# Kernel tuning notes

Hardware: AMD Instinct MI355X
Metric: run time of the kernel (lower is better)

Reference implementation:

```python
import jax, jax.numpy as jnp
import numpy as np

NX = NY = 2048
DT = 0.01
DX = 1.0
DY = 1.0
RE = 1.0
NLEVEL = int(np.log2(NY)) + 1  # 12 levels


def pad_zero(x):
    # Dirichlet (zero) halo of width 1: matches boundary_condition_u/v/k/cw
    return jnp.pad(x, ((0, 0), (0, 0), (1, 1), (1, 1)))


def pad_edge(x):
    # Edge-replicate halo (incl. corners): matches boundary_condition_p
    return jnp.pad(x, ((0, 0), (0, 0), (1, 1), (1, 1)), mode='edge')


def conv2d(x, w, stride=1):
    return jax.lax.conv_general_dilated(
        x, w, (stride, stride), 'VALID',
        dimension_numbers=('NCHW', 'OIHW', 'NCHW'))


def upsample2(x):
    return jnp.repeat(jnp.repeat(x, 2, axis=2), 2, axis=3)


def pg_vector(u, v, pad_u, pad_v, k1, ADx_u, ADy_u, ADx_v, ADy_v, AD2_u, AD2_v, w_diff):
    # Petrov-Galerkin dissipation. pad_u/pad_v are the padded ORIGINAL velocities:
    # the torch code references the global values_uu/values_vv buffers here.
    k_u = 0.25 * DX * jnp.abs(0.5 * DX ** -3 * (jnp.abs(u) * DX + jnp.abs(v) * DY) * AD2_u) \
        / (0.001 + (jnp.abs(ADx_u) * DX ** -3 + jnp.abs(ADy_u) * DX ** -3) / 2.0)
    k_v = 0.25 * DY * jnp.abs(0.5 * DX ** -3 * (jnp.abs(u) * DX + jnp.abs(v) * DY) * AD2_v) \
        / (0.001 + (jnp.abs(ADx_v) * DX ** -3 + jnp.abs(ADy_v) * DX ** -3) / 2.0)
    k_u = jnp.minimum(k_u, k1)
    k_v = jnp.minimum(k_v, k1)
    k_uu = pad_zero(k_u)
    k_vv = pad_zero(k_v)
    k_x = 1.5 * (k_u * AD2_u + conv2d(pad_u * k_uu, w_diff) - u * conv2d(k_uu, w_diff))
    k_y = 1.5 * (k_v * AD2_v + conv2d(pad_v * k_vv, w_diff) - v * conv2d(k_vv, w_diff))
    return k_x, k_y


def f_cycle_mg(pad_u, pad_v, values_p, iteration, w_A, w_res, w_xadv, w_yadv):
    diag = w_A[0, 0, 1, 1]
    b = -(conv2d(pad_u, w_xadv) + conv2d(pad_v, w_yadv)) / DT
    w = jnp.zeros((1, 1, 2, 2), values_p.dtype)
    r = b
    for _ in range(iteration):
        w = jnp.zeros((1, 1, 2, 2), values_p.dtype)
        r = conv2d(pad_edge(values_p), w_A) - b
        r_s = [r]
        for _i in range(1, NLEVEL - 1):
            r = conv2d(r, w_res, stride=2)  # restriction down to 2x2
            r_s.append(r)
        for i in reversed(range(1, NLEVEL - 1)):
            w = w - conv2d(pad_zero(w), w_A) / diag + r_s[i] / diag  # Jacobi smooth
            w = upsample2(w)  # prolongation
        values_p = values_p - w
        values_p = values_p - conv2d(pad_edge(values_p), w_A) / diag + b / diag
    return values_p, w, r


def setup_inputs() -> dict:
    key = jax.random.key(0)
    ku, kv, kp = jax.random.split(key, 3)
    shp = (1, 1, NY, NX)
    f32 = jnp.float32
    values_u = jax.random.normal(ku, shp, f32) * 0.1
    values_v = jax.random.normal(kv, shp, f32) * 0.1
    values_p = jax.random.normal(kp, shp, f32) * 0.1
    Fx = jnp.zeros(shp, f32)
    Fy = jnp.zeros(shp, f32)
    k1 = jnp.ones(shp, f32) * (DX ** 2 / DT)
    # FD stencils (learned conv params in the torch module)
    w_xadv = jnp.array([[0., 0., 0.], [-0.5, 0., 0.5], [0., 0., 0.]], f32).reshape(1, 1, 3, 3) / DX
    w_yadv = jnp.array([[0., -0.5, 0.], [0., 0., 0.], [0., 0.5, 0.]], f32).reshape(1, 1, 3, 3) / DY
    lap = jnp.array([[0., 1., 0.], [1., -4., 1.], [0., 1., 0.]], f32).reshape(1, 1, 3, 3) / DX ** 2
    w_diff = lap
    w_A = lap  # diag = -4
    w_res = jnp.full((1, 1, 2, 2), 0.25, f32)
    return dict(values_u=values_u, values_v=values_v, values_p=values_p,
                Fx=Fx, Fy=Fy, k1=k1,
                w_xadv=w_xadv, w_yadv=w_yadv, w_diff=w_diff, w_A=w_A, w_res=w_res,
                iteration=5)


def reference(values_u, values_v, values_p, Fx, Fy, k1,
              w_xadv, w_yadv, w_diff, w_A, w_res, iteration):
    pad_u = pad_zero(values_u)
    pad_v = pad_zero(values_v)
    pad_p = pad_edge(values_p)
    Grapx_p = conv2d(pad_p, w_xadv) * DT
    Grapy_p = conv2d(pad_p, w_yadv) * DT
    ADx_u = conv2d(pad_u, w_xadv); ADy_u = conv2d(pad_u, w_yadv)
    ADx_v = conv2d(pad_v, w_xadv); ADy_v = conv2d(pad_v, w_yadv)
    AD2_u = conv2d(pad_u, w_diff); AD2_v = conv2d(pad_v, w_diff)
    k_x, k_y = pg_vector(values_u, values_v, pad_u, pad_v, k1,
                         ADx_u, ADy_u, ADx_v, ADy_v, AD2_u, AD2_v, w_diff)
    b_u = values_u + 0.5 * (RE * k_x * DT - values_u * ADx_u * DT - values_v * ADy_u * DT) - Grapx_p - Fx * DT * 0
    b_v = values_v + 0.5 * (RE * k_y * DT - values_u * ADx_v * DT - values_v * ADy_v * DT) - Grapy_p - Fy * DT * 0
    pad_bu = pad_zero(b_u)
    pad_bv = pad_zero(b_v)
    ADx_u = conv2d(pad_bu, w_xadv); ADy_u = conv2d(pad_bu, w_yadv)
    ADx_v = conv2d(pad_bv, w_xadv); ADy_v = conv2d(pad_bv, w_yadv)
    AD2_u = conv2d(pad_bu, w_diff); AD2_v = conv2d(pad_bv, w_diff)
    # torch code closes over the global padded ORIGINAL velocities here (pad_u, pad_v)
    k_x, k_y = pg_vector(b_u, b_v, pad_u, pad_v, k1,
                         ADx_u, ADy_u, ADx_v, ADy_v, AD2_u, AD2_v, w_diff)
    values_u = values_u + RE * k_x * DT - b_u * ADx_u * DT - b_v * ADy_u * DT - Grapx_p - Fx * DT
    values_v = values_v + RE * k_y * DT - b_u * ADx_v * DT - b_v * ADy_v * DT - Grapy_p - Fy * DT
    values_p, w, r = f_cycle_mg(pad_zero(values_u), pad_zero(values_v), values_p,
                                iteration, w_A, w_res, w_xadv, w_yadv)
    pad_p2 = pad_edge(values_p)
    values_u = values_u - conv2d(pad_p2, w_xadv) * DT
    values_v = values_v - conv2d(pad_p2, w_yadv) * DT
    return values_u, values_v, values_p, w, r
```

## Files before the change

kernel.cpp:

```cpp
#include <hip/hip_runtime.h>

#define NN 2048
#define NN2 (NN * NN)

__device__ __forceinline__ void load6z(const float* __restrict__ A, int i, int j0, float a[6]) {
    if ((unsigned)i >= (unsigned)NN) {
#pragma unroll
        for (int q = 0; q < 6; ++q) a[q] = 0.f;
        return;
    }
    const float* row = A + (size_t)i * NN;
    float4 c = *reinterpret_cast<const float4*>(row + j0);
    a[1] = c.x; a[2] = c.y; a[3] = c.z; a[4] = c.w;
    a[0] = (j0 > 0) ? row[j0 - 1] : 0.f;
    a[5] = (j0 + 4 < NN) ? row[j0 + 4] : 0.f;
}
__device__ __forceinline__ void load4z(const float* __restrict__ A, int i, int j0, float a[4]) {
    if ((unsigned)i >= (unsigned)NN) {
#pragma unroll
        for (int q = 0; q < 4; ++q) a[q] = 0.f;
        return;
    }
    float4 c = *reinterpret_cast<const float4*>(A + (size_t)i * NN + j0);
    a[0] = c.x; a[1] = c.y; a[2] = c.z; a[3] = c.w;
}
__device__ __forceinline__ void load6e(const float* __restrict__ A, int i, int j0, float a[6]) {
    i = i < 0 ? 0 : (i > NN - 1 ? NN - 1 : i);
    const float* row = A + (size_t)i * NN;
    float4 c = *reinterpret_cast<const float4*>(row + j0);
    a[1] = c.x; a[2] = c.y; a[3] = c.z; a[4] = c.w;
    a[0] = (j0 > 0) ? row[j0 - 1] : c.x;
    a[5] = (j0 + 4 < NN) ? row[j0 + 4] : c.w;
}
__device__ __forceinline__ void load4e(const float* __restrict__ A, int i, int j0, float a[4]) {
    i = i < 0 ? 0 : (i > NN - 1 ? NN - 1 : i);
    float4 c = *reinterpret_cast<const float4*>(A + (size_t)i * NN + j0);
    a[0] = c.x; a[1] = c.y; a[2] = c.z; a[3] = c.w;
}
__device__ __forceinline__ void store4(float* __restrict__ A, int i, int j0, const float a[4]) {
    *reinterpret_cast<float4*>(A + (size_t)i * NN + j0) = make_float4(a[0], a[1], a[2], a[3]);
}

__global__ __launch_bounds__(256) void k_pred_f(const float* __restrict__ u, const float* __restrict__ v,
                                                const float* __restrict__ k1, const float* __restrict__ p,
                                                float* __restrict__ bu, float* __restrict__ bv) {
    const float DT = 0.01f;
    __shared__ __align__(16) float su[20][72], sv[20][72];
    __shared__ float sku[18][68], skv[18][68];
    const int jb = blockIdx.x * 64;
    const int ib = blockIdx.y * 16;
    const int tid = threadIdx.y * 16 + threadIdx.x;

    for (int idx = tid; idx < 20 * 18; idx += 256) {
        int r = idx / 18, c4 = idx - r * 18;
        int gi = ib - 2 + r;
        int gj = jb - 4 + c4 * 4;
        float4 uu = make_float4(0.f, 0.f, 0.f, 0.f), vv = uu;
        if ((unsigned)gi < (unsigned)NN) {
            if (gj >= 0 && gj + 3 < NN) {
                uu = *reinterpret_cast<const float4*>(u + (size_t)gi * NN + gj);
                vv = *reinterpret_cast<const float4*>(v + (size_t)gi * NN + gj);
            } else {
                float tu[4], tv[4];
#pragma unroll
                for (int q = 0; q < 4; ++q) {
                    int g = gj + q;
                    bool in = (unsigned)g < (unsigned)NN;
                    tu[q] = in ? u[(size_t)gi * NN + g] : 0.f;
                    tv[q] = in ? v[(size_t)gi * NN + g] : 0.f;
                }
                uu = make_float4(tu[0], tu[1], tu[2], tu[3]);
                vv = make_float4(tv[0], tv[1], tv[2], tv[3]);
            }
        }
        *reinterpret_cast<float4*>(&su[r][c4 * 4]) = uu;
        *reinterpret_cast<float4*>(&sv[r][c4 * 4]) = vv;
    }
    __syncthreads();

    for (int idx = tid; idx < 18 * 66; idx += 256) {
        int r = idx / 66, c = idx - r * 66;
        int gi = ib - 1 + r, gj = jb - 1 + c;
        float kuo = 0.f, kvo = 0.f;
        if ((unsigned)gi < (unsigned)NN && (unsigned)gj < (unsigned)NN) {
            int lr = r + 1, lc = c + 3;
            float uc = su[lr][lc], ul = su[lr][lc - 1], ur = su[lr][lc + 1], ut = su[lr - 1][lc], ub = su[lr + 1][lc];
            float vc = sv[lr][lc], vl = sv[lr][lc - 1], vr = sv[lr][lc + 1], vt = sv[lr - 1][lc], vb = sv[lr + 1][lc];
            float ADxu = 0.5f * (ur - ul), ADyu = 0.5f * (ub - ut);
            float ADxv = 0.5f * (vr - vl), ADyv = 0.5f * (vb - vt);
            float Lu = ul + ur + ut + ub - 4.f * uc;
            float Lv = vl + vr + vt + vb - 4.f * vc;
            float s = fabsf(uc) + fabsf(vc);
            float kuv = 0.25f * fabsf(0.5f * s * Lu) / (0.001f + 0.5f * (fabsf(ADxu) + fabsf(ADyu)));
            float kvv = 0.25f * fabsf(0.5f * s * Lv) / (0.001f + 0.5f * (fabsf(ADxv) + fabsf(ADyv)));
            float k1c = k1[(size_t)gi * NN + gj];
            kuo = fminf(kuv, k1c);
            kvo = fminf(kvv, k1c);
        }
        sku[r][c] = kuo;
        skv[r][c] = kvo;
    }
    __syncthreads();

    const int i = ib + threadIdx.y;
    const int j0 = jb + threadIdx.x * 4;
    float p6[6], pu[4], pd[4], obu[4], obv[4];
    load6e(p, i, j0, p6); load4e(p, i - 1, j0, pu); load4e(p, i + 1, j0, pd);
    const int lur = threadIdx.y + 2, lkr = threadIdx.y + 1;
#pragma unroll
    for (int c = 0; c < 4; ++c) {
        int luc = threadIdx.x * 4 + c + 4, lkc = threadIdx.x * 4 + c + 1;
        float uc = su[lur][luc], ul = su[lur][luc - 1], ur = su[lur][luc + 1], ut = su[lur - 1][luc], ub = su[lur + 1][luc];
        float vc = sv[lur][luc], vl = sv[lur][luc - 1], vr = sv[lur][luc + 1], vt = sv[lur - 1][luc], vb = sv[lur + 1][luc];
        float kuc = sku[lkr][lkc], kul = sku[lkr][lkc - 1], kur = sku[lkr][lkc + 1], kut = sku[lkr - 1][lkc], kub = sku[lkr + 1][lkc];
        float kvc = skv[lkr][lkc], kvl = skv[lkr][lkc - 1], kvr = skv[lkr][lkc + 1], kvt = skv[lkr - 1][lkc], kvb = skv[lkr + 1][lkc];
        float ADxu = 0.5f * (ur - ul), ADyu = 0.5f * (ub - ut);
        float ADxv = 0.5f * (vr - vl), ADyv = 0.5f * (vb - vt);
        float Lu = ul + ur + ut + ub - 4.f * uc;
        float Lv = vl + vr + vt + vb - 4.f * vc;
        float Lku = kul + kur + kut + kub - 4.f * kuc;
        float Lkv = kvl + kvr + kvt + kvb - 4.f * kvc;
        float Luku = ul * kul + ur * kur + ut * kut + ub * kub - 4.f * uc * kuc;
        float Lvkv = vl * kvl + vr * kvr + vt * kvt + vb * kvb - 4.f * vc * kvc;
        float kx = 1.5f * (kuc * Lu + Luku - uc * Lku);
        float ky = 1.5f * (kvc * Lv + Lvkv - vc * Lkv);
        float Grapx = 0.5f * (p6[c + 2] - p6[c]) * DT;
        float Grapy = 0.5f * (pd[c] - pu[c]) * DT;
        obu[c] = uc + 0.5f * (kx * DT - uc * ADxu * DT - vc * ADyu * DT) - Grapx;
        obv[c] = vc + 0.5f * (ky * DT - uc * ADxv * DT - vc * ADyv * DT) - Grapy;
    }
    store4(bu, i, j0, obu);
    store4(bv, i, j0, obv);
}

__global__ __launch_bounds__(256) void k_corr_f(const float* __restrict__ u, const float* __restrict__ v,
                                                const float* __restrict__ k1, const float* __restrict__ p,
                                                const float* __restrict__ bu, const float* __restrict__ bv,
                                                const float* __restrict__ Fx, const float* __restrict__ Fy,
                                                float* __restrict__ un, float* __restrict__ vn) {
    const float DT = 0.01f;
    __shared__ __align__(16) float sbu[20][72], sbv[20][72];
    __shared__ float sku[18][68], skv[18][68];
    const int jb = blockIdx.x * 64;
    const int ib = blockIdx.y * 16;
    const int tid = threadIdx.y * 16 + threadIdx.x;

    for (int idx = tid; idx < 20 * 18; idx += 256) {
        int r = idx / 18, c4 = idx - r * 18;
        int gi = ib - 2 + r;
        int gj = jb - 4 + c4 * 4;
        float4 uu = make_float4(0.f, 0.f, 0.f, 0.f), vv = uu;
        if ((unsigned)gi < (unsigned)NN) {
            if (gj >= 0 && gj + 3 < NN) {
                uu = *reinterpret_cast<const float4*>(bu + (size_t)gi * NN + gj);
                vv = *reinterpret_cast<const float4*>(bv + (size_t)gi * NN + gj);
            } else {
                float tu[4], tv[4];
#pragma unroll
                for (int q = 0; q < 4; ++q) {
                    int g = gj + q;
                    bool in = (unsigned)g < (unsigned)NN;
                    tu[q] = in ? bu[(size_t)gi * NN + g] : 0.f;
                    tv[q] = in ? bv[(size_t)gi * NN + g] : 0.f;
                }
                uu = make_float4(tu[0], tu[1], tu[2], tu[3]);
                vv = make_float4(tv[0], tv[1], tv[2], tv[3]);
            }
        }
        *reinterpret_cast<float4*>(&sbu[r][c4 * 4]) = uu;
        *reinterpret_cast<float4*>(&sbv[r][c4 * 4]) = vv;
    }
    __syncthreads();

    for (int idx = tid; idx < 18 * 66; idx += 256) {
        int r = idx / 66, c = idx - r * 66;
        int gi = ib - 1 + r, gj = jb - 1 + c;
        float kuo = 0.f, kvo = 0.f;
        if ((unsigned)gi < (unsigned)NN && (unsigned)gj < (unsigned)NN) {
            int lr = r + 1, lc = c + 3;
            float uc = sbu[lr][lc], ul = sbu[lr][lc - 1], ur = sbu[lr][lc + 1], ut = sbu[lr - 1][lc], ub = sbu[lr + 1][lc];
            float vc = sbv[lr][lc], vl = sbv[lr][lc - 1], vr = sbv[lr][lc + 1], vt = sbv[lr - 1][lc], vb = sbv[lr + 1][lc];
            float ADxu = 0.5f * (ur - ul), ADyu = 0.5f * (ub - ut);
            float ADxv = 0.5f * (vr - vl), ADyv = 0.5f * (vb - vt);
            float Lu = ul + ur + ut + ub - 4.f * uc;
            float Lv = vl + vr + vt + vb - 4.f * vc;
            float s = fabsf(uc) + fabsf(vc);
            float kuv = 0.25f * fabsf(0.5f * s * Lu) / (0.001f + 0.5f * (fabsf(ADxu) + fabsf(ADyu)));
            float kvv = 0.25f * fabsf(0.5f * s * Lv) / (0.001f + 0.5f * (fabsf(ADxv) + fabsf(ADyv)));
            float k1c = k1[(size_t)gi * NN + gj];
            kuo = fminf(kuv, k1c);
            kvo = fminf(kvv, k1c);
        }
        sku[r][c] = kuo;
        skv[r][c] = kvo;
    }
    __syncthreads();

    const int i = ib + threadIdx.y;
    const int j0 = jb + threadIdx.x * 4;
    float p6[6], pu[4], pd[4];
    float u6[6], uu[4], ud[4], v6[6], vu[4], vd[4], fx[4], fy[4], oun[4], ovn[4];
    load6e(p, i, j0, p6); load4e(p, i - 1, j0, pu); load4e(p, i + 1, j0, pd);
    load6z(u, i, j0, u6); load4z(u, i - 1, j0, uu); load4z(u, i + 1, j0, ud);
    load6z(v, i, j0, v6); load4z(v, i - 1, j0, vu); load4z(v, i + 1, j0, vd);
    load4z(Fx, i, j0, fx); load4z(Fy, i, j0, fy);
    const int lbr = threadIdx.y + 2, lkr = threadIdx.y + 1;
#pragma unroll
    for (int c = 0; c < 4; ++c) {
        int lbc = threadIdx.x * 4 + c + 4, lkc = threadIdx.x * 4 + c + 1;
        float buc = sbu[lbr][lbc], bul = sbu[lbr][lbc - 1], bur = sbu[lbr][lbc + 1], but = sbu[lbr - 1][lbc], bub = sbu[lbr + 1][lbc];
        float bvc = sbv[lbr][lbc], bvl = sbv[lbr][lbc - 1], bvr = sbv[lbr][lbc + 1], bvt = sbv[lbr - 1][lbc], bvb = sbv[lbr + 1][lbc];
        float kuc = sku[lkr][lkc], kul = sku[lkr][lkc - 1], kur = sku[lkr][lkc + 1], kut = sku[lkr - 1][lkc], kub = sku[lkr + 1][lkc];
        float kvc = skv[lkr][lkc], kvl = skv[lkr][lkc - 1], kvr = skv[lkr][lkc + 1], kvt = skv[lkr - 1][lkc], kvb = skv[lkr + 1][lkc];
        float uc = u6[c + 1], ul = u6[c], ur = u6[c + 2], ut = uu[c], ub = ud[c];
        float vc = v6[c + 1], vl = v6[c], vr = v6[c + 2], vt = vu[c], vb = vd[c];
        float ADxbu = 0.5f * (bur - bul), ADybu = 0.5f * (bub - but);
        float ADxbv = 0.5f * (bvr - bvl), ADybv = 0.5f * (bvb - bvt);
        float Lbu = bul + bur + but + bub - 4.f * buc;
        float Lbv = bvl + bvr + bvt + bvb - 4.f * bvc;
        float Lku = kul + kur + kut + kub - 4.f * kuc;
        float Lkv = kvl + kvr + kvt + kvb - 4.f * kvc;
        float Luku = ul * kul + ur * kur + ut * kut + ub * kub - 4.f * uc * kuc;
        float Lvkv = vl * kvl + vr * kvr + vt * kvt + vb * kvb - 4.f * vc * kvc;
        float kx = 1.5f * (kuc * Lbu + Luku - buc * Lku);
        float ky = 1.5f * (kvc * Lbv + Lvkv - bvc * Lkv);
        float Grapx = 0.5f * (p6[c + 2] - p6[c]) * DT;
        float Grapy = 0.5f * (pd[c] - pu[c]) * DT;
        oun[c] = uc + kx * DT - buc * ADxbu * DT - bvc * ADybu * DT - Grapx - fx[c] * DT;
        ovn[c] = vc + ky * DT - buc * ADxbv * DT - bvc * ADybv * DT - Grapy - fy[c] * DT;
    }
    store4(un, i, j0, oun);
    store4(vn, i, j0, ovn);
}

__global__ __launch_bounds__(256) void k_rhs_res(const float* __restrict__ un, const float* __restrict__ vn,
                                                 const float* __restrict__ p, float* __restrict__ b,
                                                 float* __restrict__ r1024, float* __restrict__ r512,
                                                 float* __restrict__ r256) {
    __shared__ float s512r[4][64];
    int tx = threadIdx.x, ty = threadIdx.y;
    int jt = blockIdx.x * 64 + tx;
    int it = blockIdx.y * 4 + ty;
    int j0 = jt * 4, i0 = it * 4;
    float bb[4][4];
#pragma unroll
    for (int r = 0; r < 4; ++r) {
        float u6[6], vu[4], vd[4];
        load6z(un, i0 + r, j0, u6);
        load4z(vn, i0 + r - 1, j0, vu);
        load4z(vn, i0 + r + 1, j0, vd);
#pragma unroll
        for (int c = 0; c < 4; ++c)
            bb[r][c] = -100.f * (0.5f * (u6[c + 2] - u6[c]) + 0.5f * (vd[c] - vu[c]));
        store4(b, i0 + r, j0, bb[r]);
    }
    float p6[6][6];
#pragma unroll
    for (int r = 0; r < 6; ++r) load6e(p, i0 - 1 + r, j0, p6[r]);
    float res[4][4];
#pragma unroll
    for (int r = 0; r < 4; ++r)
#pragma unroll
        for (int c = 0; c < 4; ++c) {
            float pc = p6[r + 1][c + 1];
            res[r][c] = p6[r][c + 1] + p6[r + 2][c + 1] + p6[r + 1][c] + p6[r + 1][c + 2] - 4.f * pc - bb[r][c];
        }
    float q00 = 0.25f * (res[0][0] + res[0][1] + res[1][0] + res[1][1]);
    float q01 = 0.25f * (res[0][2] + res[0][3] + res[1][2] + res[1][3]);
    float q10 = 0.25f * (res[2][0] + res[2][1] + res[3][0] + res[3][1]);
    float q11 = 0.25f * (res[2][2] + res[2][3] + res[3][2] + res[3][3]);
    int ci = it * 2, cj = jt * 2;
    *reinterpret_cast<float2*>(r1024 + (size_t)ci * 1024 + cj)       = make_float2(q00, q01);
    *reinterpret_cast<float2*>(r1024 + (size_t)(ci + 1) * 1024 + cj) = make_float2(q10, q11);
    float s = 0.25f * (q00 + q01 + q10 + q11);
    r512[(size_t)it * 512 + jt] = s;
    s512r[ty][tx] = s;
    __syncthreads();
    int tid = ty * 64 + tx;
    if (tid < 64) {
        int a = tid >> 5, c = tid & 31;
        float m = 0.25f * (s512r[2 * a][2 * c] + s512r[2 * a][2 * c + 1] + s512r[2 * a + 1][2 * c] + s512r[2 * a + 1][2 * c + 1]);
        r256[(size_t)(blockIdx.y * 2 + a) * 256 + blockIdx.x * 32 + c] = m;
    }
}

__global__ __launch_bounds__(1024) void k_small2(const float* __restrict__ r256in,
                                                 float* __restrict__ r128g,
                                                 float* __restrict__ w128_out,
                                                 float* __restrict__ r2_out) {
    __shared__ float sr128[128 * 128];
    __shared__ float sr64[64 * 64];
    __shared__ float sr32[32 * 32];
    __shared__ float sr16[16 * 16];
    __shared__ float sr8[8 * 8];
    __shared__ float sr4[16];
    __shared__ float sr2[4];
    __shared__ float wa[64 * 64];
    __shared__ float wb[64 * 64];
    int t = threadIdx.x;

    for (int idx = t; idx < 128 * 128; idx += 1024) {
        int i = idx >> 7, j = idx & 127;
        const float* s0 = r256in + (2 * i) * 256 + 2 * j;
        float m = 0.25f * (s0[0] + s0[1] + s0[256] + s0[257]);
        sr128[idx] = m;
        r128g[idx] = m;
    }
    __syncthreads();
    for (int idx = t; idx < 64 * 64; idx += 1024) {
        int i = idx >> 6, j = idx & 63;
        const float* s0 = sr128 + (2 * i) * 128 + 2 * j;
        sr64[idx] = 0.25f * (s0[0] + s0[1] + s0[128] + s0[129]);
    }
    __syncthreads();
    if (t < 32 * 32) {
        int i = t >> 5, j = t & 31;
        const float* s0 = sr64 + (2 * i) * 64 + 2 * j;
        sr32[t] = 0.25f * (s0[0] + s0[1] + s0[64] + s0[65]);
    }
    __syncthreads();
    if (t < 16 * 16) {
        int i = t >> 4, j = t & 15;
        const float* s0 = sr32 + (2 * i) * 32 + 2 * j;
        sr16[t] = 0.25f * (s0[0] + s0[1] + s0[32] + s0[33]);
    }
    __syncthreads();
    if (t < 64) {
        int i = t >> 3, j = t & 7;
        const float* s0 = sr16 + (2 * i) * 16 + 2 * j;
        sr8[t] = 0.25f * (s0[0] + s0[1] + s0[16] + s0[17]);
    }
    __syncthreads();
    if (t < 16) {
        int i = t >> 2, j = t & 3;
        const float* s0 = sr8 + (2 * i) * 8 + 2 * j;
        sr4[t] = 0.25f * (s0[0] + s0[1] + s0[8] + s0[9]);
    }
    __syncthreads();
    if (t < 4) {
        int i = t >> 1, j = t & 1;
        const float* s0 = sr4 + (2 * i) * 4 + 2 * j;
        sr2[t] = 0.25f * (s0[0] + s0[1] + s0[4] + s0[5]);
        r2_out[t] = sr2[t];
        float ws = -0.25f * sr2[t];
        wa[(2 * i) * 4 + 2 * j] = ws;
        wa[(2 * i) * 4 + 2 * j + 1] = ws;
        wa[(2 * i + 1) * 4 + 2 * j] = ws;
        wa[(2 * i + 1) * 4 + 2 * j + 1] = ws;
    }
    __syncthreads();

    auto step = [&](const float* win, const float* rl, float* wout, int s) {
        for (int idx = t; idx < s * s; idx += 1024) {
            int i = idx / s, j = idx - i * s;
            float up = i > 0 ? win[(i - 1) * s + j] : 0.f;
            float dn = i < s - 1 ? win[(i + 1) * s + j] : 0.f;
            float lf = j > 0 ? win[i * s + j - 1] : 0.f;
            float rt = j < s - 1 ? win[i * s + j + 1] : 0.f;
            float ws = 0.25f * (up + dn + lf + rt - rl[idx]);
            int o = 2 * s;
            wout[(2 * i) * o + 2 * j] = ws;
            wout[(2 * i) * o + 2 * j + 1] = ws;
            wout[(2 * i + 1) * o + 2 * j] = ws;
            wout[(2 * i + 1) * o + 2 * j + 1] = ws;
        }
    };
    step(wa, sr4, wb, 4);
    __syncthreads();
    step(wb, sr8, wa, 8);
    __syncthreads();
    step(wa, sr16, wb, 16);
    __syncthreads();
    step(wb, sr32, wa, 32);
    __syncthreads();
    step(wa, sr64, w128_out, 64);
}

__global__ __launch_bounds__(256) void k_prolong2(const float* __restrict__ w128, const float* __restrict__ r128,
                                                  const float* __restrict__ r256, float* __restrict__ w512) {
    __shared__ float sw[5][68];
    __shared__ float s128[3][66];
    __shared__ float s256[2][128];
    const int jb = blockIdx.x * 256;
    const int ob = blockIdx.y * 4;
    const int by = blockIdx.y;
    const int rw = by - 2, cw = jb / 4 - 2;
    const int rs = by - 1, cs = jb / 4 - 1;
    const int tid = threadIdx.y * 64 + threadIdx.x;

    for (int idx = tid; idx < 5 * 68; idx += 256) {
        int r = idx / 68, c = idx - r * 68;
        int x = rw + r, y = cw + c;
        sw[r][c] = ((unsigned)x < 128u && (unsigned)y < 128u) ? w128[x * 128 + y] : 0.f;
    }
    __syncthreads();
    if (tid < 3 * 66) {
        int r = tid / 66, c = tid - (tid / 66) * 66;
        int x = rs + r, y = cs + c;
        float val = 0.f;
        if ((unsigned)x < 128u && (unsigned)y < 128u) {
            int lr = r + 1, lc = c + 1;
            val = 0.25f * (sw[lr - 1][lc] + sw[lr + 1][lc] + sw[lr][lc - 1] + sw[lr][lc + 1] - r128[x * 128 + y]);
        }
        s128[r][c] = val;
    }
    __syncthreads();
    {
        int rr = tid >> 7, cc = tid & 127;
        int X = 2 * by + rr, Y = jb / 2 + cc;
        float s = 0.f;
        if (X > 0)   s += s128[((X - 1) >> 1) - rs][(Y >> 1) - cs];
        if (X < 255) s += s128[((X + 1) >> 1) - rs][(Y >> 1) - cs];
        if (Y > 0)   s += s128[(X >> 1) - rs][((Y - 1) >> 1) - cs];
        if (Y < 255) s += s128[(X >> 1) - rs][((Y + 1) >> 1) - cs];
        s256[rr][cc] = 0.25f * (s - r256[X * 256 + Y]);
    }
    __syncthreads();
    const int i = ob + threadIdx.y;
    const int j0 = jb + threadIdx.x * 4;
    const int lr = (i >> 1) - 2 * by;
    float o[4];
#pragma unroll
    for (int c = 0; c < 4; ++c) o[c] = s256[lr][((j0 + c) >> 1) - jb / 2];
    *reinterpret_cast<float4*>(w512 + (size_t)i * 512 + j0) = make_float4(o[0], o[1], o[2], o[3]);
}

template <bool LAST>
__global__ __launch_bounds__(256) void k_pupd3(
    const float* __restrict__ p, const float* __restrict__ b,
    const float* __restrict__ w512, const float* __restrict__ r512,
    const float* __restrict__ r1024,
    float* __restrict__ pdst,
    float* __restrict__ o1024, float* __restrict__ o512, float* __restrict__ o256,
    float* __restrict__ wout, float* __restrict__ un, float* __restrict__ vn)
{
    __shared__ float sW[6][38];
    __shared__ float sS[4][36];
    __shared__ float ws[6][68];
    __shared__ __align__(16) float pmid[12][136];
    __shared__ float pnew[10][130];
    __shared__ float sq[4][64];
    __shared__ float red[2][32];

    const int jb = blockIdx.x * 128;
    const int ib = blockIdx.y * 8;
    const int tid = threadIdx.y * 32 + threadIdx.x;
    const int r1 = ib / 2 - 1, c1 = jb / 2 - 2;
    const int r2 = ib / 4 - 1, c2 = jb / 4 - 2;
    const int r3 = ib / 4 - 2, c3 = jb / 4 - 3;

    for (int idx = tid; idx < 6 * 38; idx += 256) {
        int r = idx / 38, c = idx - r * 38;
        int x = r3 + r, y = c3 + c;
        sW[r][c] = ((unsigned)x < 512u && (unsigned)y < 512u) ? w512[(size_t)x * 512 + y] : 0.f;
    }
    __syncthreads();
    if (tid < 4 * 36) {
        int r = tid / 36, c = tid - (tid / 36) * 36;
        int x = r2 + r, y = c2 + c;
        float val = 0.f;
        if ((unsigned)x < 512u && (unsigned)y < 512u) {
            int lr = r + 1, lc = c + 1;
            val = 0.25f * (sW[lr - 1][lc] + sW[lr + 1][lc] + sW[lr][lc - 1] + sW[lr][lc + 1]
                           - r512[(size_t)x * 512 + y]);
        }
        sS[r][c] = val;
    }
    __syncthreads();
    for (int idx = tid; idx < 6 * 68; idx += 256) {
        int r = idx / 68, c = idx - r * 68;
        int x = r1 + r, y = c1 + c;
        float val = 0.f;
        if ((unsigned)x < 1024u && (unsigned)y < 1024u) {
            float s = 0.f;
            if (x > 0)    s += sS[((x - 1) >> 1) - r2][(y >> 1) - c2];
            if (x < 1023) s += sS[((x + 1) >> 1) - r2][(y >> 1) - c2];
            if (y > 0)    s += sS[(x >> 1) - r2][((y - 1) >> 1) - c2];
            if (y < 1023) s += sS[(x >> 1) - r2][((y + 1) >> 1) - c2];
            val = 0.25f * (s - r1024[(size_t)x * 1024 + y]);
        }
        ws[r][c] = val;
    }
    __syncthreads();
    for (int idx = tid; idx < 12 * 34; idx += 256) {
        int r = idx / 34, q = idx - r * 34;
        int gi = ib - 2 + r;
        int gj0 = jb - 4 + q * 4;
        float vals[4] = {0.f, 0.f, 0.f, 0.f};
        if ((unsigned)gi < (unsigned)NN) {
            if (gj0 >= 0 && gj0 + 3 < NN) {
                float4 pv = *reinterpret_cast<const float4*>(p + (size_t)gi * NN + gj0);
                vals[0] = pv.x; vals[1] = pv.y; vals[2] = pv.z; vals[3] = pv.w;
            } else {
#pragma unroll
                for (int q4 = 0; q4 < 4; ++q4) {
                    int gj = gj0 + q4;
                    vals[q4] = ((unsigned)gj < (unsigned)NN) ? p[(size_t)gi * NN + gj] : 0.f;
                }
            }
        }
#pragma unroll
        for (int q4 = 0; q4 < 4; ++q4) {
            int gj = gj0 + q4;
            float m = 0.f;
            if ((unsigned)gi < (unsigned)NN && (unsigned)gj < (unsigned)NN &&
                gj >= jb - 2 && gj <= jb + 129) {
                m = vals[q4] - ws[(gi >> 1) - r1][(gj >> 1) - c1];
            }
            pmid[r][q * 4 + q4] = m;
        }
    }
    __syncthreads();
    for (int idx = tid; idx < 10 * 130; idx += 256) {
        int r = idx / 130, c = idx - r * 130;
        int gi = ib - 1 + r, gj = jb - 1 + c;
        float val = 0.f;
        if ((unsigned)gi < (unsigned)NN && (unsigned)gj < (unsigned)NN) {
            int iu = gi > 0 ? gi - 1 : 0;
            int idn = gi < NN - 1 ? gi + 1 : NN - 1;
            int jl = gj > 0 ? gj - 1 : 0;
            int jr = gj < NN - 1 ? gj + 1 : NN - 1;
            float s = pmid[iu - (ib - 2)][gj - (jb - 4)] + pmid[idn - (ib - 2)][gj - (jb - 4)]
                    + pmid[gi - (ib - 2)][jl - (jb - 4)] + pmid[gi - (ib - 2)][jr - (jb - 4)];
            val = 0.25f * (s - b[(size_t)gi * NN + gj]);
        }
        pnew[r][c] = val;
    }
    __syncthreads();

    const int i  = ib + threadIdx.y;
    const int j0 = jb + threadIdx.x * 4;
    const int lr = i - (ib - 1);
    const int lc = j0 - (jb - 1);
    *reinterpret_cast<float4*>(pdst + (size_t)i * NN + j0) =
        make_float4(pnew[lr][lc], pnew[lr][lc + 1], pnew[lr][lc + 2], pnew[lr][lc + 3]);

    if (LAST) {
        const float DT = 0.01f;
        float ow[4];
        int wr = (i >> 1) - r1;
#pragma unroll
        for (int c = 0; c < 4; ++c) ow[c] = ws[wr][((j0 + c) >> 1) - c1];
        store4(wout, i, j0, ow);
        float4 uu = *reinterpret_cast<float4*>(un + (size_t)i * NN + j0);
        float4 vv = *reinterpret_cast<float4*>(vn + (size_t)i * NN + j0);
        float ou[4] = {uu.x, uu.y, uu.z, uu.w};
        float ov[4] = {vv.x, vv.y, vv.z, vv.w};
        int iu = (i > 0 ? i - 1 : 0) - (ib - 1);
        int idn = (i < NN - 1 ? i + 1 : NN - 1) - (ib - 1);
#pragma unroll
        for (int c = 0; c < 4; ++c) {
            int j = j0 + c;
            int jl = (j > 0 ? j - 1 : 0) - (jb - 1);
            int jr = (j < NN - 1 ? j + 1 : NN - 1) - (jb - 1);
            int lcc = j - (jb - 1);
            ou[c] -= 0.5f * (pnew[lr][jr] - pnew[lr][jl]) * DT;
            ov[c] -= 0.5f * (pnew[idn][lcc] - pnew[iu][lcc]) * DT;
        }
        store4(un, i, j0, ou);
        store4(vn, i, j0, ov);
    } else {
        int cr = tid >> 6, cc = tid & 63;
        float q = 0.f;
#pragma unroll
        for (int dr = 0; dr < 2; ++dr) {
#pragma unroll
            for (int dc = 0; dc < 2; ++dc) {
                int i2 = ib + 2 * cr + dr, j2 = jb + 2 * cc + dc;
                int lr2 = i2 - (ib - 1), lc2 = j2 - (jb - 1);
                int iu2 = (i2 > 0 ? i2 - 1 : 0) - (ib - 1);
                int id2 = (i2 < NN - 1 ? i2 + 1 : NN - 1) - (ib - 1);
                int jl2 = (j2 > 0 ? j2 - 1 : 0) - (jb - 1);
                int jr2 = (j2 < NN - 1 ? j2 + 1 : NN - 1) - (jb - 1);
                q += pnew[iu2][lc2] + pnew[id2][lc2] + pnew[lr2][jl2] + pnew[lr2][jr2]
                   - 4.f * pnew[lr2][lc2] - b[(size_t)i2 * NN + j2];
            }
        }
        q *= 0.25f;
        sq[cr][cc] = q;
        o1024[(size_t)(ib / 2 + cr) * 1024 + jb / 2 + cc] = q;
        __syncthreads();
        if (tid < 64) {
            int rr = tid >> 5, c5 = tid & 31;
            float m = 0.25f * (sq[2 * rr][2 * c5] + sq[2 * rr][2 * c5 + 1] +
                               sq[2 * rr + 1][2 * c5] + sq[2 * rr + 1][2 * c5 + 1]);
            o512[(size_t)(ib / 4 + rr) * 512 + jb / 4 + c5] = m;
            red[rr][c5] = m;
        }
        __syncthreads();
        if (tid < 16) {
            float m = 0.25f * (red[0][2 * tid] + red[0][2 * tid + 1] +
                               red[1][2 * tid] + red[1][2 * tid + 1]);
            o256[(size_t)(ib / 8) * 256 + jb / 8 + tid] = m;
        }
    }
}

extern "C" void kernel_launch(void* const* d_in, const int* in_sizes, int n_in,
                              void* d_out, int out_size, void* d_ws, size_t ws_size,
                              hipStream_t stream) {
    const float* u  = (const float*)d_in[0];
    const float* v  = (const float*)d_in[1];
    const float* p  = (const float*)d_in[2];
    const float* Fx = (const float*)d_in[3];
    const float* Fy = (const float*)d_in[4];
    const float* k1 = (const float*)d_in[5];

    float* out = (float*)d_out;
    float* out_u = out;
    float* out_v = out + (size_t)NN2;
    float* out_p = out + 2 * (size_t)NN2;
    float* out_w = out + 3 * (size_t)NN2;
    float* out_r = out + 4 * (size_t)NN2;

    float* wsb = (float*)d_ws;
    float* b  = wsb;
    float* pA = wsb + (size_t)NN2;
    float* pB = wsb + 2 * (size_t)NN2;
    float* base = wsb + 3 * (size_t)NN2;
    float* rA1024 = base;
    float* rA512  = rA1024 + 1024 * 1024;
    float* rA256  = rA512 + 512 * 512;
    float* rB1024 = rA256 + 256 * 256;
    float* rB512  = rB1024 + 1024 * 1024;
    float* rB256  = rB512 + 512 * 512;
    float* r128   = rB256 + 256 * 256;
    float* w128   = r128 + 128 * 128;
    float* w512   = w128 + 128 * 128;

    float* bu = out_w;
    float* bv = out_p;

    dim3 blkT(16, 16);
    dim3 gT(32, 128);
    dim3 blkR(64, 4);
    dim3 gR(8, 128);
    dim3 blkP(32, 8);
    dim3 gP(16, 256);
    dim3 gL(2, 128);

    k_pred_f<<<gT, blkT, 0, stream>>>(u, v, k1, p, bu, bv);
    k_corr_f<<<gT, blkT, 0, stream>>>(u, v, k1, p, bu, bv, Fx, Fy, out_u, out_v);
    k_rhs_res<<<gR, blkR, 0, stream>>>(out_u, out_v, p, b, rA1024, rA512, rA256);

    const float* pcur = p;
    for (int it = 0; it < 5; ++it) {
        const bool useA = (it % 2 == 0);
        const float* R1024 = useA ? rA1024 : rB1024;
        const float* R512  = useA ? rA512  : rB512;
        const float* R256  = useA ? rA256  : rB256;
        float* O1024 = useA ? rB1024 : rA1024;
        float* O512  = useA ? rB512  : rA512;
        float* O256  = useA ? rB256  : rA256;

        k_small2<<<1, 1024, 0, stream>>>(R256, r128, w128, out_r);
        k_prolong2<<<gL, blkR, 0, stream>>>(w128, r128, R256, w512);
        if (it < 4) {
            float* pdst = (it & 1) ? pB : pA;
            k_pupd3<false><<<gP, blkP, 0, stream>>>(pcur, b, w512, R512, R1024,
                                                    pdst, O1024, O512, O256,
                                                    nullptr, nullptr, nullptr);
            pcur = pdst;
        } else {
            k_pupd3<true><<<gP, blkP, 0, stream>>>(pcur, b, w512, R512, R1024,
                                                   out_p, nullptr, nullptr, nullptr,
                                                   out_w, out_u, out_v);
        }
    }
}
```

Before: 393.1 us.

## Fuse prolongation levels into p-update kernel and move 128 restriction upstream

Removes the separate k_prolong2 launch per V-cycle by computing the 128->256->512 prolongation and smoothing on the fly inside a new k_pupd5 kernel, using 16-row tiles with each thread handling two rows. The 256->128 restriction moves out of k_small into k_rhs_res and the p-update kernel, so k_small reads r128 directly. This saves one launch per iteration and the w512 round trip through global memory, at the cost of redundant halo computation per block and more shared memory. Shared arrays are also padded to odd strides, which replaces float4 shared stores with scalar stores.

```diff
diff --git a/kernel.cpp b/kernel.cpp
--- a/kernel.cpp
+++ b/kernel.cpp
@@ -45,8 +45,8 @@
                                                 const float* __restrict__ k1, const float* __restrict__ p,
                                                 float* __restrict__ bu, float* __restrict__ bv) {
     const float DT = 0.01f;
-    __shared__ __align__(16) float su[20][72], sv[20][72];
-    __shared__ float sku[18][68], skv[18][68];
+    __shared__ float su[20][73], sv[20][73];
+    __shared__ float sku[18][69], skv[18][69];
     const int jb = blockIdx.x * 64;
     const int ib = blockIdx.y * 16;
     const int tid = threadIdx.y * 16 + threadIdx.x;
@@ -55,26 +55,26 @@
         int r = idx / 18, c4 = idx - r * 18;
         int gi = ib - 2 + r;
         int gj = jb - 4 + c4 * 4;
-        float4 uu = make_float4(0.f, 0.f, 0.f, 0.f), vv = uu;
+        float tu[4] = {0.f, 0.f, 0.f, 0.f}, tv[4] = {0.f, 0.f, 0.f, 0.f};
         if ((unsigned)gi < (unsigned)NN) {
             if (gj >= 0 && gj + 3 < NN) {
-                uu = *reinterpret_cast<const float4*>(u + (size_t)gi * NN + gj);
-                vv = *reinterpret_cast<const float4*>(v + (size_t)gi * NN + gj);
+                float4 a = *reinterpret_cast<const float4*>(u + (size_t)gi * NN + gj);
+                float4 bq = *reinterpret_cast<const float4*>(v + (size_t)gi * NN + gj);
+                tu[0] = a.x; tu[1] = a.y; tu[2] = a.z; tu[3] = a.w;
+                tv[0] = bq.x; tv[1] = bq.y; tv[2] = bq.z; tv[3] = bq.w;
             } else {
-                float tu[4], tv[4];
 #pragma unroll
                 for (int q = 0; q < 4; ++q) {
                     int g = gj + q;
-                    bool in = (unsigned)g < (unsigned)NN;
-                    tu[q] = in ? u[(size_t)gi * NN + g] : 0.f;
-                    tv[q] = in ? v[(size_t)gi * NN + g] : 0.f;
+                    if ((unsigned)g < (unsigned)NN) {
+                        tu[q] = u[(size_t)gi * NN + g];
+                        tv[q] = v[(size_t)gi * NN + g];
+                    }
                 }
-                uu = make_float4(tu[0], tu[1], tu[2], tu[3]);
-                vv = make_float4(tv[0], tv[1], tv[2], tv[3]);
             }
         }
-        *reinterpret_cast<float4*>(&su[r][c4 * 4]) = uu;
-        *reinterpret_cast<float4*>(&sv[r][c4 * 4]) = vv;
+#pragma unroll
+        for (int q = 0; q < 4; ++q) { su[r][c4 * 4 + q] = tu[q]; sv[r][c4 * 4 + q] = tv[q]; }
     }
     __syncthreads();
 
@@ -139,8 +139,8 @@
                                                 const float* __restrict__ Fx, const float* __restrict__ Fy,
                                                 float* __restrict__ un, float* __restrict__ vn) {
     const float DT = 0.01f;
-    __shared__ __align__(16) float sbu[20][72], sbv[20][72];
-    __shared__ float sku[18][68], skv[18][68];
+    __shared__ float sbu[20][73], sbv[20][73];
+    __shared__ float sku[18][69], skv[18][69];
     const int jb = blockIdx.x * 64;
     const int ib = blockIdx.y * 16;
     const int tid = threadIdx.y * 16 + threadIdx.x;
@@ -149,26 +149,26 @@
         int r = idx / 18, c4 = idx - r * 18;
         int gi = ib - 2 + r;
         int gj = jb - 4 + c4 * 4;
-        float4 uu = make_float4(0.f, 0.f, 0.f, 0.f), vv = uu;
+        float tu[4] = {0.f, 0.f, 0.f, 0.f}, tv[4] = {0.f, 0.f, 0.f, 0.f};
         if ((unsigned)gi < (unsigned)NN) {
             if (gj >= 0 && gj + 3 < NN) {
-                uu = *reinterpret_cast<const float4*>(bu + (size_t)gi * NN + gj);
-                vv = *reinterpret_cast<const float4*>(bv + (size_t)gi * NN + gj);
+                float4 a = *reinterpret_cast<const float4*>(bu + (size_t)gi * NN + gj);
+                float4 bq = *reinterpret_cast<const float4*>(bv + (size_t)gi * NN + gj);
+                tu[0] = a.x; tu[1] = a.y; tu[2] = a.z; tu[3] = a.w;
+                tv[0] = bq.x; tv[1] = bq.y; tv[2] = bq.z; tv[3] = bq.w;
             } else {
-                float tu[4], tv[4];
 #pragma unroll
                 for (int q = 0; q < 4; ++q) {
                     int g = gj + q;
-                    bool in = (unsigned)g < (unsigned)NN;
-                    tu[q] = in ? bu[(size_t)gi * NN + g] : 0.f;
-                    tv[q] = in ? bv[(size_t)gi * NN + g] : 0.f;
+                    if ((unsigned)g < (unsigned)NN) {
+                        tu[q] = bu[(size_t)gi * NN + g];
+                        tv[q] = bv[(size_t)gi * NN + g];
+                    }
                 }
-                uu = make_float4(tu[0], tu[1], tu[2], tu[3]);
-                vv = make_float4(tv[0], tv[1], tv[2], tv[3]);
             }
         }
-        *reinterpret_cast<float4*>(&sbu[r][c4 * 4]) = uu;
-        *reinterpret_cast<float4*>(&sbv[r][c4 * 4]) = vv;
+#pragma unroll
+        for (int q = 0; q < 4; ++q) { sbu[r][c4 * 4 + q] = tu[q]; sbv[r][c4 * 4 + q] = tv[q]; }
     }
     __syncthreads();
 
@@ -236,8 +236,9 @@
 __global__ __launch_bounds__(256) void k_rhs_res(const float* __restrict__ un, const float* __restrict__ vn,
                                                  const float* __restrict__ p, float* __restrict__ b,
                                                  float* __restrict__ r1024, float* __restrict__ r512,
-                                                 float* __restrict__ r256) {
-    __shared__ float s512r[4][64];
+                                                 float* __restrict__ r256, float* __restrict__ r128) {
+    __shared__ float s512r[4][65];
+    __shared__ float s256r[2][33];
     int tx = threadIdx.x, ty = threadIdx.y;
     int jt = blockIdx.x * 64 + tx;
     int it = blockIdx.y * 4 + ty;
@@ -281,14 +282,18 @@
         int a = tid >> 5, c = tid & 31;
         float m = 0.25f * (s512r[2 * a][2 * c] + s512r[2 * a][2 * c + 1] + s512r[2 * a + 1][2 * c] + s512r[2 * a + 1][2 * c + 1]);
         r256[(size_t)(blockIdx.y * 2 + a) * 256 + blockIdx.x * 32 + c] = m;
-    }
-}
-
-__global__ __launch_bounds__(1024) void k_small2(const float* __restrict__ r256in,
-                                                 float* __restrict__ r128g,
-                                                 float* __restrict__ w128_out,
-                                                 float* __restrict__ r2_out) {
-    __shared__ float sr128[128 * 128];
+        s256r[a][c] = m;
+    }
+    __syncthreads();
+    if (tid < 16) {
+        float m = 0.25f * (s256r[0][2 * tid] + s256r[0][2 * tid + 1] + s256r[1][2 * tid] + s256r[1][2 * tid + 1]);
+        r128[(size_t)blockIdx.y * 128 + blockIdx.x * 16 + tid] = m;
+    }
+}
+
+__global__ __launch_bounds__(1024) void k_small(const float* __restrict__ r128,
+                                                float* __restrict__ w128_out,
+                                                float* __restrict__ r2_out) {
     __shared__ float sr64[64 * 64];
     __shared__ float sr32[32 * 32];
     __shared__ float sr16[16 * 16];
@@ -299,17 +304,9 @@
     __shared__ float wb[64 * 64];
     int t = threadIdx.x;
 
-    for (int idx = t; idx < 128 * 128; idx += 1024) {
-        int i = idx >> 7, j = idx & 127;
-        const float* s0 = r256in + (2 * i) * 256 + 2 * j;
-        float m = 0.25f * (s0[0] + s0[1] + s0[256] + s0[257]);
-        sr128[idx] = m;
-        r128g[idx] = m;
-    }
-    __syncthreads();
     for (int idx = t; idx < 64 * 64; idx += 1024) {
         int i = idx >> 6, j = idx & 63;
-        const float* s0 = sr128 + (2 * i) * 128 + 2 * j;
+        const float* s0 = r128 + (2 * i) * 128 + 2 * j;
         sr64[idx] = 0.25f * (s0[0] + s0[1] + s0[128] + s0[129]);
     }
     __syncthreads();
@@ -376,98 +373,90 @@
     step(wa, sr64, w128_out, 64);
 }
 
-__global__ __launch_bounds__(256) void k_prolong2(const float* __restrict__ w128, const float* __restrict__ r128,
-                                                  const float* __restrict__ r256, float* __restrict__ w512) {
-    __shared__ float sw[5][68];
-    __shared__ float s128[3][66];
-    __shared__ float s256[2][128];
-    const int jb = blockIdx.x * 256;
-    const int ob = blockIdx.y * 4;
-    const int by = blockIdx.y;
-    const int rw = by - 2, cw = jb / 4 - 2;
-    const int rs = by - 1, cs = jb / 4 - 1;
-    const int tid = threadIdx.y * 64 + threadIdx.x;
-
-    for (int idx = tid; idx < 5 * 68; idx += 256) {
-        int r = idx / 68, c = idx - r * 68;
-        int x = rw + r, y = cw + c;
+template <bool LAST>
+__global__ __launch_bounds__(256) void k_pupd5(
+    const float* __restrict__ p, const float* __restrict__ b,
+    const float* __restrict__ w128, const float* __restrict__ r128,
+    const float* __restrict__ r256, const float* __restrict__ r512,
+    const float* __restrict__ r1024,
+    float* __restrict__ pdst,
+    float* __restrict__ o1024, float* __restrict__ o512,
+    float* __restrict__ o256, float* __restrict__ o128,
+    float* __restrict__ wout, float* __restrict__ un, float* __restrict__ vn)
+{
+    __shared__ float sw[5][15];
+    __shared__ float s128[3][13];
+    __shared__ float s256[4][21];
+    __shared__ float sS[6][37];
+    __shared__ float ws[10][69];
+    __shared__ float pmid[20][137];
+    __shared__ float pnew[18][131];
+    __shared__ float sq[8][65];
+    __shared__ float red[4][33];
+    __shared__ float red2[2][17];
+
+    const int jb = blockIdx.x * 128;
+    const int ib = blockIdx.y * 16;
+    const int tid = threadIdx.y * 32 + threadIdx.x;
+    const int r1 = ib / 2 - 1,  c1 = jb / 2 - 2;
+    const int r2 = ib / 4 - 1,  c2 = jb / 4 - 2;
+    const int r3 = ib / 8 - 1,  c3 = jb / 8 - 2;
+    const int r4 = ib / 16 - 1, c4 = jb / 16 - 2;
+    const int r5 = ib / 16 - 2, c5 = jb / 16 - 3;
+
+    if (tid < 5 * 14) {
+        int r = tid / 14, c = tid - (tid / 14) * 14;
+        int x = r5 + r, y = c5 + c;
         sw[r][c] = ((unsigned)x < 128u && (unsigned)y < 128u) ? w128[x * 128 + y] : 0.f;
     }
     __syncthreads();
-    if (tid < 3 * 66) {
-        int r = tid / 66, c = tid - (tid / 66) * 66;
-        int x = rs + r, y = cs + c;
+    if (tid < 3 * 12) {
+        int r = tid / 12, c = tid - (tid / 12) * 12;
+        int x = r4 + r, y = c4 + c;
         float val = 0.f;
         if ((unsigned)x < 128u && (unsigned)y < 128u) {
-            int lr = r + 1, lc = c + 1;
-            val = 0.25f * (sw[lr - 1][lc] + sw[lr + 1][lc] + sw[lr][lc - 1] + sw[lr][lc + 1] - r128[x * 128 + y]);
+            int lr = x - r5, lc = y - c5;
+            float s = 0.f;
+            if (x > 0)   s += sw[lr - 1][lc];
+            if (x < 127) s += sw[lr + 1][lc];
+            if (y > 0)   s += sw[lr][lc - 1];
+            if (y < 127) s += sw[lr][lc + 1];
+            val = 0.25f * (s - r128[x * 128 + y]);
         }
         s128[r][c] = val;
     }
     __syncthreads();
-    {
-        int rr = tid >> 7, cc = tid & 127;
-        int X = 2 * by + rr, Y = jb / 2 + cc;
-        float s = 0.f;
-        if (X > 0)   s += s128[((X - 1) >> 1) - rs][(Y >> 1) - cs];
-        if (X < 255) s += s128[((X + 1) >> 1) - rs][(Y >> 1) - cs];
-        if (Y > 0)   s += s128[(X >> 1) - rs][((Y - 1) >> 1) - cs];
-        if (Y < 255) s += s128[(X >> 1) - rs][((Y + 1) >> 1) - cs];
-        s256[rr][cc] = 0.25f * (s - r256[X * 256 + Y]);
-    }
-    __syncthreads();
-    const int i = ob + threadIdx.y;
-    const int j0 = jb + threadIdx.x * 4;
-    const int lr = (i >> 1) - 2 * by;
-    float o[4];
-#pragma unroll
-    for (int c = 0; c < 4; ++c) o[c] = s256[lr][((j0 + c) >> 1) - jb / 2];
-    *reinterpret_cast<float4*>(w512 + (size_t)i * 512 + j0) = make_float4(o[0], o[1], o[2], o[3]);
-}
-
-template <bool LAST>
-__global__ __launch_bounds__(256) void k_pupd3(
-    const float* __restrict__ p, const float* __restrict__ b,
-    const float* __restrict__ w512, const float* __restrict__ r512,
-    const float* __restrict__ r1024,
-    float* __restrict__ pdst,
-    float* __restrict__ o1024, float* __restrict__ o512, float* __restrict__ o256,
-    float* __restrict__ wout, float* __restrict__ un, float* __restrict__ vn)
-{
-    __shared__ float sW[6][38];
-    __shared__ float sS[4][36];
-    __shared__ float ws[6][68];
-    __shared__ __align__(16) float pmid[12][136];
-    __shared__ float pnew[10][130];
-    __shared__ float sq[4][64];
-    __shared__ float red[2][32];
-
-    const int jb = blockIdx.x * 128;
-    const int ib = blockIdx.y * 8;
-    const int tid = threadIdx.y * 32 + threadIdx.x;
-    const int r1 = ib / 2 - 1, c1 = jb / 2 - 2;
-    const int r2 = ib / 4 - 1, c2 = jb / 4 - 2;
-    const int r3 = ib / 4 - 2, c3 = jb / 4 - 3;
-
-    for (int idx = tid; idx < 6 * 38; idx += 256) {
-        int r = idx / 38, c = idx - r * 38;
+    if (tid < 4 * 20) {
+        int r = tid / 20, c = tid - (tid / 20) * 20;
         int x = r3 + r, y = c3 + c;
-        sW[r][c] = ((unsigned)x < 512u && (unsigned)y < 512u) ? w512[(size_t)x * 512 + y] : 0.f;
-    }
-    __syncthreads();
-    if (tid < 4 * 36) {
+        float val = 0.f;
+        if ((unsigned)x < 256u && (unsigned)y < 256u) {
+            float s = 0.f;
+            if (x > 0)   s += s128[((x - 1) >> 1) - r4][(y >> 1) - c4];
+            if (x < 255) s += s128[((x + 1) >> 1) - r4][(y >> 1) - c4];
+            if (y > 0)   s += s128[(x >> 1) - r4][((y - 1) >> 1) - c4];
+            if (y < 255) s += s128[(x >> 1) - r4][((y + 1) >> 1) - c4];
+            val = 0.25f * (s - r256[x * 256 + y]);
+        }
+        s256[r][c] = val;
+    }
+    __syncthreads();
+    if (tid < 6 * 36) {
         int r = tid / 36, c = tid - (tid / 36) * 36;
         int x = r2 + r, y = c2 + c;
         float val = 0.f;
         if ((unsigned)x < 512u && (unsigned)y < 512u) {
-            int lr = r + 1, lc = c + 1;
-            val = 0.25f * (sW[lr - 1][lc] + sW[lr + 1][lc] + sW[lr][lc - 1] + sW[lr][lc + 1]
-                           - r512[(size_t)x * 512 + y]);
+            float s = 0.f;
+            if (x > 0)   s += s256[((x - 1) >> 1) - r3][(y >> 1) - c3];
+            if (x < 511) s += s256[((x + 1) >> 1) - r3][(y >> 1) - c3];
+            if (y > 0)   s += s256[(x >> 1) - r3][((y - 1) >> 1) - c3];
+            if (y < 511) s += s256[(x >> 1) - r3][((y + 1) >> 1) - c3];
+            val = 0.25f * (s - r512[(size_t)x * 512 + y]);
         }
         sS[r][c] = val;
     }
     __syncthreads();
-    for (int idx = tid; idx < 6 * 68; idx += 256) {
+    for (int idx = tid; idx < 10 * 68; idx += 256) {
         int r = idx / 68, c = idx - r * 68;
         int x = r1 + r, y = c1 + c;
         float val = 0.f;
@@ -482,7 +471,7 @@
         ws[r][c] = val;
     }
     __syncthreads();
-    for (int idx = tid; idx < 12 * 34; idx += 256) {
+    for (int idx = tid; idx < 20 * 34; idx += 256) {
         int r = idx / 34, q = idx - r * 34;
         int gi = ib - 2 + r;
         int gj0 = jb - 4 + q * 4;
@@ -511,7 +500,7 @@
         }
     }
     __syncthreads();
-    for (int idx = tid; idx < 10 * 130; idx += 256) {
+    for (int idx = tid; idx < 18 * 130; idx += 256) {
         int r = idx / 130, c = idx - r * 130;
         int gi = ib - 1 + r, gj = jb - 1 + c;
         float val = 0.f;
@@ -528,70 +517,90 @@
     }
     __syncthreads();
 
-    const int i  = ib + threadIdx.y;
     const int j0 = jb + threadIdx.x * 4;
-    const int lr = i - (ib - 1);
-    const int lc = j0 - (jb - 1);
-    *reinterpret_cast<float4*>(pdst + (size_t)i * NN + j0) =
-        make_float4(pnew[lr][lc], pnew[lr][lc + 1], pnew[lr][lc + 2], pnew[lr][lc + 3]);
+#pragma unroll
+    for (int rr = 0; rr < 2; ++rr) {
+        int i = ib + threadIdx.y + rr * 8;
+        int lr = i - (ib - 1);
+        int lc = j0 - (jb - 1);
+        *reinterpret_cast<float4*>(pdst + (size_t)i * NN + j0) =
+            make_float4(pnew[lr][lc], pnew[lr][lc + 1], pnew[lr][lc + 2], pnew[lr][lc + 3]);
+    }
 
     if (LAST) {
         const float DT = 0.01f;
-        float ow[4];
-        int wr = (i >> 1) - r1;
-#pragma unroll
-        for (int c = 0; c < 4; ++c) ow[c] = ws[wr][((j0 + c) >> 1) - c1];
-        store4(wout, i, j0, ow);
-        float4 uu = *reinterpret_cast<float4*>(un + (size_t)i * NN + j0);
-        float4 vv = *reinterpret_cast<float4*>(vn + (size_t)i * NN + j0);
-        float ou[4] = {uu.x, uu.y, uu.z, uu.w};
-        float ov[4] = {vv.x, vv.y, vv.z, vv.w};
-        int iu = (i > 0 ? i - 1 : 0) - (ib - 1);
-        int idn = (i < NN - 1 ? i + 1 : NN - 1) - (ib - 1);
-#pragma unroll
-        for (int c = 0; c < 4; ++c) {
-            int j = j0 + c;
-            int jl = (j > 0 ? j - 1 : 0) - (jb - 1);
-            int jr = (j < NN - 1 ? j + 1 : NN - 1) - (jb - 1);
-            int lcc = j - (jb - 1);
-            ou[c] -= 0.5f * (pnew[lr][jr] - pnew[lr][jl]) * DT;
-            ov[c] -= 0.5f * (pnew[idn][lcc] - pnew[iu][lcc]) * DT;
-        }
-        store4(un, i, j0, ou);
-        store4(vn, i, j0, ov);
+#pragma unroll
+        for (int rr = 0; rr < 2; ++rr) {
+            int i = ib + threadIdx.y + rr * 8;
+            int lr = i - (ib - 1);
+            int wr = (i >> 1) - r1;
+            float ow[4];
+#pragma unroll
+            for (int c = 0; c < 4; ++c) ow[c] = ws[wr][((j0 + c) >> 1) - c1];
+            store4(wout, i, j0, ow);
+            float4 uu = *reinterpret_cast<float4*>(un + (size_t)i * NN + j0);
+            float4 vv = *reinterpret_cast<float4*>(vn + (size_t)i * NN + j0);
+            float ou[4] = {uu.x, uu.y, uu.z, uu.w};
+            float ov[4] = {vv.x, vv.y, vv.z, vv.w};
+            int iu = (i > 0 ? i - 1 : 0) - (ib - 1);
+            int idn = (i < NN - 1 ? i + 1 : NN - 1) - (ib - 1);
+#pragma unroll
+            for (int c = 0; c < 4; ++c) {
+                int j = j0 + c;
+                int jl = (j > 0 ? j - 1 : 0) - (jb - 1);
+                int jr = (j < NN - 1 ? j + 1 : NN - 1) - (jb - 1);
+                int lcc = j - (jb - 1);
+                ou[c] -= 0.5f * (pnew[lr][jr] - pnew[lr][jl]) * DT;
+                ov[c] -= 0.5f * (pnew[idn][lcc] - pnew[iu][lcc]) * DT;
+            }
+            store4(un, i, j0, ou);
+            store4(vn, i, j0, ov);
+        }
     } else {
-        int cr = tid >> 6, cc = tid & 63;
-        float q = 0.f;
-#pragma unroll
-        for (int dr = 0; dr < 2; ++dr) {
-#pragma unroll
-            for (int dc = 0; dc < 2; ++dc) {
-                int i2 = ib + 2 * cr + dr, j2 = jb + 2 * cc + dc;
-                int lr2 = i2 - (ib - 1), lc2 = j2 - (jb - 1);
-                int iu2 = (i2 > 0 ? i2 - 1 : 0) - (ib - 1);
-                int id2 = (i2 < NN - 1 ? i2 + 1 : NN - 1) - (ib - 1);
-                int jl2 = (j2 > 0 ? j2 - 1 : 0) - (jb - 1);
-                int jr2 = (j2 < NN - 1 ? j2 + 1 : NN - 1) - (jb - 1);
-                q += pnew[iu2][lc2] + pnew[id2][lc2] + pnew[lr2][jl2] + pnew[lr2][jr2]
-                   - 4.f * pnew[lr2][lc2] - b[(size_t)i2 * NN + j2];
+#pragma unroll
+        for (int rr = 0; rr < 2; ++rr) {
+            int cr = (tid >> 6) + rr * 4;
+            int cc = tid & 63;
+            float q = 0.f;
+#pragma unroll
+            for (int dr = 0; dr < 2; ++dr) {
+#pragma unroll
+                for (int dc = 0; dc < 2; ++dc) {
+                    int i2 = ib + 2 * cr + dr, j2 = jb + 2 * cc + dc;
+                    int lr2 = i2 - (ib - 1), lc2 = j2 - (jb - 1);
+                    int iu2 = (i2 > 0 ? i2 - 1 : 0) - (ib - 1);
+                    int id2 = (i2 < NN - 1 ? i2 + 1 : NN - 1) - (ib - 1);
+                    int jl2 = (j2 > 0 ? j2 - 1 : 0) - (jb - 1);
+                    int jr2 = (j2 < NN - 1 ? j2 + 1 : NN - 1) - (jb - 1);
+                    q += pnew[iu2][lc2] + pnew[id2][lc2] + pnew[lr2][jl2] + pnew[lr2][jr2]
+                       - 4.f * pnew[lr2][lc2] - b[(size_t)i2 * NN + j2];
+                }
             }
-        }
-        q *= 0.25f;
-        sq[cr][cc] = q;
-        o1024[(size_t)(ib / 2 + cr) * 1024 + jb / 2 + cc] = q;
+            q *= 0.25f;
+            sq[cr][cc] = q;
+            o1024[(size_t)(ib / 2 + cr) * 1024 + jb / 2 + cc] = q;
+        }
         __syncthreads();
-        if (tid < 64) {
-            int rr = tid >> 5, c5 = tid & 31;
-            float m = 0.25f * (sq[2 * rr][2 * c5] + sq[2 * rr][2 * c5 + 1] +
-                               sq[2 * rr + 1][2 * c5] + sq[2 * rr + 1][2 * c5 + 1]);
-            o512[(size_t)(ib / 4 + rr) * 512 + jb / 4 + c5] = m;
-            red[rr][c5] = m;
+        if (tid < 128) {
+            int rr = tid >> 5, cc = tid & 31;
+            float m = 0.25f * (sq[2 * rr][2 * cc] + sq[2 * rr][2 * cc + 1] +
+                               sq[2 * rr + 1][2 * cc] + sq[2 * rr + 1][2 * cc + 1]);
+            o512[(size_t)(ib / 4 + rr) * 512 + jb / 4 + cc] = m;
+            red[rr][cc] = m;
         }
         __syncthreads();
-        if (tid < 16) {
-            float m = 0.25f * (red[0][2 * tid] + red[0][2 * tid + 1] +
-                               red[1][2 * tid] + red[1][2 * tid + 1]);
-            o256[(size_t)(ib / 8) * 256 + jb / 8 + tid] = m;
+        if (tid < 32) {
+            int rr = tid >> 4, cc = tid & 15;
+            float m = 0.25f * (red[2 * rr][2 * cc] + red[2 * rr][2 * cc + 1] +
+                               red[2 * rr + 1][2 * cc] + red[2 * rr + 1][2 * cc + 1]);
+            o256[(size_t)(ib / 8 + rr) * 256 + jb / 8 + cc] = m;
+            red2[rr][cc] = m;
+        }
+        __syncthreads();
+        if (tid < 8) {
+            float m = 0.25f * (red2[0][2 * tid] + red2[0][2 * tid + 1] +
+                               red2[1][2 * tid] + red2[1][2 * tid + 1]);
+            o128[(size_t)(ib / 16) * 128 + jb / 16 + tid] = m;
         }
     }
 }
@@ -621,12 +630,12 @@
     float* rA1024 = base;
     float* rA512  = rA1024 + 1024 * 1024;
     float* rA256  = rA512 + 512 * 512;
-    float* rB1024 = rA256 + 256 * 256;
+    float* rA128  = rA256 + 256 * 256;
+    float* rB1024 = rA128 + 128 * 128;
     float* rB512  = rB1024 + 1024 * 1024;
     float* rB256  = rB512 + 512 * 512;
-    float* r128   = rB256 + 256 * 256;
-    float* w128   = r128 + 128 * 128;
-    float* w512   = w128 + 128 * 128;
+    float* rB128  = rB256 + 256 * 256;
+    float* w128   = rB128 + 128 * 128;
 
     float* bu = out_w;
     float* bv = out_p;
@@ -636,12 +645,11 @@
     dim3 blkR(64, 4);
     dim3 gR(8, 128);
     dim3 blkP(32, 8);
-    dim3 gP(16, 256);
-    dim3 gL(2, 128);
+    dim3 gP(16, 128);
 
     k_pred_f<<<gT, blkT, 0, stream>>>(u, v, k1, p, bu, bv);
     k_corr_f<<<gT, blkT, 0, stream>>>(u, v, k1, p, bu, bv, Fx, Fy, out_u, out_v);
-    k_rhs_res<<<gR, blkR, 0, stream>>>(out_u, out_v, p, b, rA1024, rA512, rA256);
+    k_rhs_res<<<gR, blkR, 0, stream>>>(out_u, out_v, p, b, rA1024, rA512, rA256, rA128);
 
     const float* pcur = p;
     for (int it = 0; it < 5; ++it) {
@@ -649,21 +657,22 @@
         const float* R1024 = useA ? rA1024 : rB1024;
         const float* R512  = useA ? rA512  : rB512;
         const float* R256  = useA ? rA256  : rB256;
+        const float* R128  = useA ? rA128  : rB128;
         float* O1024 = useA ? rB1024 : rA1024;
         float* O512  = useA ? rB512  : rA512;
         float* O256  = useA ? rB256  : rA256;
-
-        k_small2<<<1, 1024, 0, stream>>>(R256, r128, w128, out_r);
-        k_prolong2<<<gL, blkR, 0, stream>>>(w128, r128, R256, w512);
+        float* O128  = useA ? rB128  : rA128;
+
+        k_small<<<1, 1024, 0, stream>>>(R128, w128, out_r);
         if (it < 4) {
             float* pdst = (it & 1) ? pB : pA;
-            k_pupd3<false><<<gP, blkP, 0, stream>>>(pcur, b, w512, R512, R1024,
-                                                    pdst, O1024, O512, O256,
+            k_pupd5<false><<<gP, blkP, 0, stream>>>(pcur, b, w128, R128, R256, R512, R1024,
+                                                    pdst, O1024, O512, O256, O128,
                                                     nullptr, nullptr, nullptr);
             pcur = pdst;
         } else {
-            k_pupd3<true><<<gP, blkP, 0, stream>>>(pcur, b, w512, R512, R1024,
-                                                   out_p, nullptr, nullptr, nullptr,
+            k_pupd5<true><<<gP, blkP, 0, stream>>>(pcur, b, w128, R128, R256, R512, R1024,
+                                                   out_p, nullptr, nullptr, nullptr, nullptr,
                                                    out_w, out_u, out_v);
         }
     }
```

Result: faster. 377.4 us (-4.0%).
